# Performance work log

Hardware: AMD Instinct MI355X
Metric: run time of the kernel (lower is better)

Reference implementation:

```python
import jax, jax.numpy as jnp
import numpy as np

NEG_SLOPE = 0.2
EPS = 1e-16  # PyG softmax eps


def _gat_conv(x, src, dst, W, att_src, att_dst, bias, heads, out_ch):
    """PyG GATConv (eval mode, self-loops already appended, concat output)."""
    N = x.shape[0]
    xw = (x @ W).reshape(N, heads, out_ch)            # [N,H,C]
    a_src = jnp.sum(xw * att_src, axis=-1)            # [N,H]
    a_dst = jnp.sum(xw * att_dst, axis=-1)            # [N,H]
    e = jax.nn.leaky_relu(a_src[src] + a_dst[dst], NEG_SLOPE)  # [E,H]
    m = jax.ops.segment_max(e, dst, num_segments=N)   # [N,H] (self-loops -> no empty segs)
    e = jnp.exp(e - m[dst])
    denom = jax.ops.segment_sum(e, dst, num_segments=N)
    alpha = e / (denom[dst] + EPS)                    # [E,H]
    msg = xw[src] * alpha[:, :, None]                 # [E,H,C]
    out = jax.ops.segment_sum(msg, dst, num_segments=N)  # [N,H,C]
    return out.reshape(N, heads * out_ch) + bias


def setup_inputs() -> dict:
    key = jax.random.key(0)
    ks = jax.random.split(key, 12)
    N, E, F_in, H, C, NC = 20000, 320000, 512, 8, 64, 32
    x = jax.random.normal(ks[0], (N, F_in), dtype=jnp.float32)
    edge_index = jax.random.randint(ks[1], (2, E), 0, N, dtype=jnp.int64)
    g = lambda k, shape, fan: jax.random.normal(k, shape, dtype=jnp.float32) * (1.0 / np.sqrt(fan))
    return {
        "x": x,
        "edge_index": edge_index,
        "W1": g(ks[2], (F_in, H * C), F_in),
        "att_src1": g(ks[3], (H, C), C),
        "att_dst1": g(ks[4], (H, C), C),
        "b1": jnp.zeros((H * C,), dtype=jnp.float32),
        "W2": g(ks[5], (H * C, NC), H * C),
        "att_src2": g(ks[6], (1, NC), NC),
        "att_dst2": g(ks[7], (1, NC), NC),
        "b2": jnp.zeros((NC,), dtype=jnp.float32),
    }


def reference(x, edge_index, W1, att_src1, att_dst1, b1, W2, att_src2, att_dst2, b2):
    N = x.shape[0]
    H, C = att_src1.shape
    NC = att_src2.shape[1]
    # GATConv adds self-loops by default
    loops = jnp.arange(N, dtype=edge_index.dtype)
    src = jnp.concatenate([edge_index[0], loops])
    dst = jnp.concatenate([edge_index[1], loops])
    h = _gat_conv(x, src, dst, W1, att_src1, att_dst1, b1, H, C)
    h = jax.nn.elu(h)
    h = _gat_conv(h, src, dst, W2, att_src2, att_dst2, b2, 1, NC)
    return jax.nn.log_softmax(h, axis=1)
```

## Files before the change

kernel.cpp:

```cpp
#include <hip/hip_runtime.h>
#include <math.h>

#define NEG_SLOPE 0.2f
#define SM_EPS 1e-16f

typedef short short8 __attribute__((ext_vector_type(8)));
typedef float floatx4 __attribute__((ext_vector_type(4)));


__device__ inline unsigned short f2bf(float x) {
    unsigned int u = __float_as_uint(x);
    unsigned int r = (u + 0x7FFFu + ((u >> 16) & 1u)) >> 16;
    return (unsigned short)r;
}

__device__ inline float bf2f(unsigned short h) {
    return __uint_as_float(((unsigned int)h) << 16);
}

__device__ inline float bflo(unsigned int u) { return __uint_as_float(u << 16); }
__device__ inline float bfhi(unsigned int u) { return __uint_as_float(u & 0xFFFF0000u); }

__device__ __forceinline__ void gl_lds16(const unsigned short* g, unsigned short* l) {
    __builtin_amdgcn_global_load_lds(
        (const __attribute__((address_space(1))) unsigned int*)(g),
        (__attribute__((address_space(3))) unsigned int*)(l), 16, 0, 0);
}

__device__ inline void get_edge(const int* __restrict__ srcA, const int* __restrict__ dstA,
                                int e, int E, int& s, int& d) {
    if (e < E) { s = srcA[e]; d = dstA[e]; }
    else { s = e - E; d = e - E; }
}


__global__ __launch_bounds__(256) void k_prep(const float* __restrict__ x,
                                              unsigned short* __restrict__ xb,
                                              const float* __restrict__ W1,
                                              unsigned short* __restrict__ w1t,
                                              const float* __restrict__ W2,
                                              unsigned short* __restrict__ w2bt,
                                              const int* __restrict__ dstA,
                                              int E, int Ep,
                                              int* __restrict__ deg,
                                              int nblk_deg, int nblk_x) {
    __shared__ float tile[32][33];
    int bx = blockIdx.x;
    int t = threadIdx.x;
    if (bx < nblk_deg) {
        int e = bx * 256 + t;
        if (e < Ep) {
            int d = (e < E) ? dstA[e] : (e - E);
            atomicAdd(&deg[d], 1);
        }
    } else if (bx < nblk_deg + nblk_x) {
        int i = ((bx - nblk_deg) * 256 + t) * 4;
        float4 v = *(const float4*)(x + i);
        ushort4 o;
        o.x = f2bf(v.x); o.y = f2bf(v.y); o.z = f2bf(v.z); o.w = f2bf(v.w);
        *(ushort4*)(xb + i) = o;
    } else if (bx < nblk_deg + nblk_x + 256) {
        int b = bx - nblk_deg - nblk_x;
        int kb = (b & 15) * 32;
        int nb = (b >> 4) * 32;
        int tx = t & 31, ty = t >> 5;
        #pragma unroll
        for (int i = 0; i < 32; i += 8)
            tile[ty + i][tx] = W1[(size_t)(kb + ty + i) * 512 + nb + tx];
        __syncthreads();
        #pragma unroll
        for (int i = 0; i < 32; i += 8)
            w1t[(size_t)(nb + ty + i) * 512 + kb + tx] = f2bf(tile[tx][ty + i]);
    } else {
        int i = (bx - nblk_deg - nblk_x - 256) * 256 + t;
        int c = i >> 9, k = i & 511;
        w2bt[i] = f2bf(W2[k * 32 + c]);
    }
}


__global__ __launch_bounds__(256) void k_scan_fused(const int* __restrict__ deg,
                                                    int* __restrict__ part,
                                                    int* __restrict__ done,
                                                    int* __restrict__ off,
                                                    int* __restrict__ cursor,
                                                    int N, int nblk) {
    __shared__ int sm[256];
    int bx = blockIdx.x, t = threadIdx.x;
    int i = bx * 256 + t;
    int v = (i < N) ? deg[i] : 0;
    sm[t] = v; __syncthreads();
    for (int o = 1; o < 256; o <<= 1) {
        int x = (t >= o) ? sm[t - o] : 0;
        __syncthreads();
        sm[t] += x;
        __syncthreads();
    }
    int incl_v = sm[t];
    if (t == 255) {
        part[bx] = sm[255];
        __threadfence();
        atomicAdd(done, 1);
    }
    if (t == 0) {
        while (atomicAdd(done, 0) < nblk) { }
        __threadfence();
    }
    __syncthreads();
    int partial = 0;
    for (int j = t; j < bx; j += 256) partial += atomicAdd(&part[j], 0);
    sm[t] = partial; __syncthreads();
    for (int o = 128; o > 0; o >>= 1) {
        if (t < o) sm[t] += sm[t + o];
        __syncthreads();
    }
    int base = sm[0];
    if (i < N) {
        int vv = incl_v + base;
        off[i + 1] = vv;
        cursor[i] = vv - v;
        if (i == 0) off[0] = 0;
    }
}

__global__ __launch_bounds__(256) void k_scatter(const int* __restrict__ srcA, const int* __restrict__ dstA,
                                                 int E, int Ep, int* __restrict__ cursor,
                                                 int* __restrict__ src_s) {
    int e = blockIdx.x * 256 + threadIdx.x;
    if (e >= Ep) return;
    int s, d; get_edge(srcA, dstA, e, E, s, d);
    int p = atomicAdd(&cursor[d], 1);
    src_s[p] = s;
}


__global__ __launch_bounds__(256, 4) void k_gemm1_mfma(const unsigned short* __restrict__ A,
                                                       const unsigned short* __restrict__ Bt,
                                                       const float* __restrict__ att_s,
                                                       const float* __restrict__ att_d,
                                                       unsigned short* __restrict__ C,
                                                       float* __restrict__ a_sd,
                                                       float* __restrict__ a_dd, int M) {
    const int K = 512;
    __shared__ unsigned short As[2][64 * 32];
    __shared__ unsigned short Bs[2][128 * 32];
    int t = threadIdx.x;
    int lane = t & 63;
    int w = t >> 6;
    int row0 = blockIdx.x * 64;
    int col0 = blockIdx.y * 128;
    int wm = (w >> 1) * 32, wn = (w & 1) * 64;
    int l15 = lane & 15, q = lane >> 4;

    int srl = lane >> 2;
    int sgc = ((lane & 3) ^ ((lane >> 3) & 3)) * 8;

    floatx4 acc[2][4] = {};

    auto STAGE = [&](int buf, int k0) {
        gl_lds16(A  + (size_t)(row0 + w * 16 + srl) * K + k0 + sgc, &As[buf][(w * 16) * 32]);
        gl_lds16(Bt + (size_t)(col0 + w * 32 + srl) * K + k0 + sgc, &Bs[buf][(w * 32) * 32]);
        gl_lds16(Bt + (size_t)(col0 + w * 32 + 16 + srl) * K + k0 + sgc, &Bs[buf][(w * 32 + 16) * 32]);
    };

    STAGE(0, 0);
    asm volatile("s_waitcnt vmcnt(0)" ::: "memory");
    __builtin_amdgcn_s_barrier();

    int swz = (l15 >> 1) & 3;
    int buf = 0;
    for (int k0 = 0; k0 < K; k0 += 32) {
        if (k0 + 32 < K) {
            STAGE(buf ^ 1, k0 + 32);
            asm volatile("s_waitcnt vmcnt(3)" ::: "memory");
        } else {
            asm volatile("s_waitcnt vmcnt(0)" ::: "memory");
        }
        __builtin_amdgcn_s_barrier();
        __builtin_amdgcn_sched_barrier(0);
        short8 af[2], bfr[4];
        int sw = (q ^ swz) << 3;
        #pragma unroll
        for (int i = 0; i < 2; ++i)
            af[i] = *(const short8*)(&As[buf][(wm + i * 16 + l15) * 32 + sw]);
        #pragma unroll
        for (int j = 0; j < 4; ++j)
            bfr[j] = *(const short8*)(&Bs[buf][(wn + j * 16 + l15) * 32 + sw]);
        #pragma unroll
        for (int i = 0; i < 2; ++i)
            #pragma unroll
            for (int j = 0; j < 4; ++j)
                acc[i][j] = __builtin_amdgcn_mfma_f32_16x16x32_bf16(af[i], bfr[j], acc[i][j], 0, 0, 0);
        asm volatile("s_waitcnt lgkmcnt(0)" ::: "memory");
        __builtin_amdgcn_sched_barrier(0);
        __builtin_amdgcn_s_barrier();
        buf ^= 1;
    }

    #pragma unroll
    for (int i = 0; i < 2; ++i) {
        #pragma unroll
        for (int p = 0; p < 4; ++p) {
            int r = row0 + wm + i * 16 + q * 4 + p;
            if (r < M) {
                #pragma unroll
                for (int j = 0; j < 4; ++j) {
                    int c = col0 + wn + j * 16 + l15;
                    C[(size_t)r * 512 + c] = f2bf(acc[i][j][p]);
                }
            }
        }
    }

    int hh = blockIdx.y * 2 + (w & 1);
    float asr[4], adr[4];
    #pragma unroll
    for (int j = 0; j < 4; ++j) {
        asr[j] = att_s[hh * 64 + j * 16 + l15];
        adr[j] = att_d[hh * 64 + j * 16 + l15];
    }
    #pragma unroll
    for (int i = 0; i < 2; ++i) {
        #pragma unroll
        for (int p = 0; p < 4; ++p) {
            float ds = 0.f, dd = 0.f;
            #pragma unroll
            for (int j = 0; j < 4; ++j) {
                ds = fmaf(acc[i][j][p], asr[j], ds);
                dd = fmaf(acc[i][j][p], adr[j], dd);
            }
            #pragma unroll
            for (int mk = 1; mk <= 8; mk <<= 1) {
                ds += __shfl_xor(ds, mk);
                dd += __shfl_xor(dd, mk);
            }
            int r = row0 + wm + i * 16 + q * 4 + p;
            if (l15 == 0 && r < M) {
                a_sd[(size_t)hh * M + r] = ds;
                a_dd[(size_t)hh * M + r] = dd;
            }
        }
    }
}


__global__ __launch_bounds__(256) void k_l1(const unsigned short* __restrict__ xw,
                                            const float* __restrict__ a_s,
                                            const float* __restrict__ a_d,
                                            const int* __restrict__ off,
                                            const int* __restrict__ src_s,
                                            const float* __restrict__ bias,
                                            unsigned short* __restrict__ hout, int N) {
    int wid = threadIdx.x >> 6, lane = threadIdx.x & 63;
    int h = blockIdx.x & 7;
    int n = (blockIdx.x >> 3) * 32 + wid * 8 + (lane >> 3);
    int li = lane & 7;
    if (n >= N) return;
    int p0 = off[n], p1 = off[n + 1];
    const float* ash = a_s + (size_t)h * N;
    float adv = a_d[(size_t)h * N + n];
    const size_t cbase = (size_t)h * 64 + (size_t)li * 8;

    float acc[8] = {};
    float s = 0.f;
    int p = p0;
    if (p + 4 <= p1) {
        int s0 = src_s[p], s1 = src_s[p + 1], s2 = src_s[p + 2], s3 = src_s[p + 3];
        while (true) {
            const uint4 u0 = *(const uint4*)(xw + (size_t)s0 * 512 + cbase);
            const uint4 u1 = *(const uint4*)(xw + (size_t)s1 * 512 + cbase);
            const uint4 u2 = *(const uint4*)(xw + (size_t)s2 * 512 + cbase);
            const uint4 u3 = *(const uint4*)(xw + (size_t)s3 * 512 + cbase);
            float e0 = ash[s0] + adv; e0 = e0 > 0.f ? e0 : NEG_SLOPE * e0;
            float e1 = ash[s1] + adv; e1 = e1 > 0.f ? e1 : NEG_SLOPE * e1;
            float e2 = ash[s2] + adv; e2 = e2 > 0.f ? e2 : NEG_SLOPE * e2;
            float e3 = ash[s3] + adv; e3 = e3 > 0.f ? e3 : NEG_SLOPE * e3;
            int np = p + 4;
            bool more = (np + 4 <= p1);
            int t0 = 0, t1 = 0, t2 = 0, t3 = 0;
            if (more) {
                t0 = src_s[np]; t1 = src_s[np + 1];
                t2 = src_s[np + 2]; t3 = src_s[np + 3];
            }
            float w0 = __expf(e0);
            float w1 = __expf(e1);
            float w2 = __expf(e2);
            float w3 = __expf(e3);
            s += (w0 + w1) + (w2 + w3);
            acc[0] = fmaf(w0, bflo(u0.x), acc[0]); acc[1] = fmaf(w0, bfhi(u0.x), acc[1]);
            acc[2] = fmaf(w0, bflo(u0.y), acc[2]); acc[3] = fmaf(w0, bfhi(u0.y), acc[3]);
            acc[4] = fmaf(w0, bflo(u0.z), acc[4]); acc[5] = fmaf(w0, bfhi(u0.z), acc[5]);
            acc[6] = fmaf(w0, bflo(u0.w), acc[6]); acc[7] = fmaf(w0, bfhi(u0.w), acc[7]);
            acc[0] = fmaf(w1, bflo(u1.x), acc[0]); acc[1] = fmaf(w1, bfhi(u1.x), acc[1]);
            acc[2] = fmaf(w1, bflo(u1.y), acc[2]); acc[3] = fmaf(w1, bfhi(u1.y), acc[3]);
            acc[4] = fmaf(w1, bflo(u1.z), acc[4]); acc[5] = fmaf(w1, bfhi(u1.z), acc[5]);
            acc[6] = fmaf(w1, bflo(u1.w), acc[6]); acc[7] = fmaf(w1, bfhi(u1.w), acc[7]);
            acc[0] = fmaf(w2, bflo(u2.x), acc[0]); acc[1] = fmaf(w2, bfhi(u2.x), acc[1]);
            acc[2] = fmaf(w2, bflo(u2.y), acc[2]); acc[3] = fmaf(w2, bfhi(u2.y), acc[3]);
            acc[4] = fmaf(w2, bflo(u2.z), acc[4]); acc[5] = fmaf(w2, bfhi(u2.z), acc[5]);
            acc[6] = fmaf(w2, bflo(u2.w), acc[6]); acc[7] = fmaf(w2, bfhi(u2.w), acc[7]);
            acc[0] = fmaf(w3, bflo(u3.x), acc[0]); acc[1] = fmaf(w3, bfhi(u3.x), acc[1]);
            acc[2] = fmaf(w3, bflo(u3.y), acc[2]); acc[3] = fmaf(w3, bfhi(u3.y), acc[3]);
            acc[4] = fmaf(w3, bflo(u3.z), acc[4]); acc[5] = fmaf(w3, bfhi(u3.z), acc[5]);
            acc[6] = fmaf(w3, bflo(u3.w), acc[6]); acc[7] = fmaf(w3, bfhi(u3.w), acc[7]);
            p = np;
            if (!more) break;
            s0 = t0; s1 = t1; s2 = t2; s3 = t3;
        }
    }
    for (; p < p1; ++p) {
        int s0 = src_s[p];
        const uint4 u0 = *(const uint4*)(xw + (size_t)s0 * 512 + cbase);
        float e0 = ash[s0] + adv; e0 = e0 > 0.f ? e0 : NEG_SLOPE * e0;
        float w0 = __expf(e0);
        s += w0;
        acc[0] = fmaf(w0, bflo(u0.x), acc[0]); acc[1] = fmaf(w0, bfhi(u0.x), acc[1]);
        acc[2] = fmaf(w0, bflo(u0.y), acc[2]); acc[3] = fmaf(w0, bfhi(u0.y), acc[3]);
        acc[4] = fmaf(w0, bflo(u0.z), acc[4]); acc[5] = fmaf(w0, bfhi(u0.z), acc[5]);
        acc[6] = fmaf(w0, bflo(u0.w), acc[6]); acc[7] = fmaf(w0, bfhi(u0.w), acc[7]);
    }

    float inv = 1.f / (s + SM_EPS);
    unsigned int ov[4];
    #pragma unroll
    for (int j = 0; j < 4; ++j) {
        float v0 = acc[2 * j] * inv     + bias[cbase + 2 * j];
        float v1 = acc[2 * j + 1] * inv + bias[cbase + 2 * j + 1];
        v0 = v0 > 0.f ? v0 : __expf(v0) - 1.f;
        v1 = v1 > 0.f ? v1 : __expf(v1) - 1.f;
        ov[j] = (unsigned int)f2bf(v0) | ((unsigned int)f2bf(v1) << 16);
    }
    *(uint4*)(hout + (size_t)n * 512 + cbase) = make_uint4(ov[0], ov[1], ov[2], ov[3]);
}


__global__ __launch_bounds__(256) void k_gemm2_mfma(const unsigned short* __restrict__ A,
                                                    const unsigned short* __restrict__ Bt,
                                                    const float* __restrict__ att_s,
                                                    const float* __restrict__ att_d,
                                                    unsigned short* __restrict__ O,
                                                    float* __restrict__ a_s, float* __restrict__ a_d,
                                                    int M) {
    const int K = 512;
    __shared__ unsigned short As[64 * 512];
    __shared__ unsigned short Bs[32 * 512];
    int t = threadIdx.x;
    int lane = t & 63;
    int w = t >> 6;
    int row0 = blockIdx.x * 64;
    int l15 = lane & 15, q = lane >> 4;

    #pragma unroll
    for (int i = 0; i < 16; ++i) {
        int r = w * 16 + i;
        gl_lds16(A + (size_t)(row0 + r) * K + ((lane ^ (r & 7)) << 3), &As[r * 512]);
    }
    #pragma unroll
    for (int i = 0; i < 8; ++i) {
        int r = w * 8 + i;
        gl_lds16(Bt + (size_t)r * K + ((lane ^ (r & 7)) << 3), &Bs[r * 512]);
    }
    __syncthreads();

    floatx4 acc[2] = {};
    int ra = w * 16 + l15;
    int rb0 = l15, rb1 = 16 + l15;
    #pragma unroll
    for (int k0 = 0; k0 < K; k0 += 32) {
        int cc = (k0 >> 3) + q;
        short8 af = *(const short8*)(&As[ra * 512 + ((cc ^ (ra & 7)) << 3)]);
        short8 b0 = *(const short8*)(&Bs[rb0 * 512 + ((cc ^ (rb0 & 7)) << 3)]);
        short8 b1 = *(const short8*)(&Bs[rb1 * 512 + ((cc ^ (rb1 & 7)) << 3)]);
        acc[0] = __builtin_amdgcn_mfma_f32_16x16x32_bf16(af, b0, acc[0], 0, 0, 0);
        acc[1] = __builtin_amdgcn_mfma_f32_16x16x32_bf16(af, b1, acc[1], 0, 0, 0);
    }

    float as_lo = att_s[l15], as_hi = att_s[16 + l15];
    float ad_lo = att_d[l15], ad_hi = att_d[16 + l15];
    #pragma unroll
    for (int p = 0; p < 4; ++p) {
        int r = row0 + w * 16 + q * 4 + p;
        bool ok = r < M;
        float v0 = acc[0][p], v1 = acc[1][p];
        if (ok) {
            O[(size_t)r * 32 + l15]      = f2bf(v0);
            O[(size_t)r * 32 + 16 + l15] = f2bf(v1);
        }
        float ds = v0 * as_lo + v1 * as_hi;
        float dd = v0 * ad_lo + v1 * ad_hi;
        #pragma unroll
        for (int mk = 1; mk <= 8; mk <<= 1) {
            ds += __shfl_xor(ds, mk);
            dd += __shfl_xor(dd, mk);
        }
        if (ok && l15 == 0) { a_s[r] = ds; a_d[r] = dd; }
    }
}


__global__ __launch_bounds__(256) void k_l2(const unsigned short* __restrict__ hw2,
                                            const float* __restrict__ a_s,
                                            const float* __restrict__ a_d,
                                            const int* __restrict__ off,
                                            const int* __restrict__ src_s,
                                            const float* __restrict__ bias,
                                            float* __restrict__ outp, int N) {
    int wid = threadIdx.x >> 6, lane = threadIdx.x & 63;
    int n = blockIdx.x * 4 + wid;
    if (n >= N) return;
    int p0 = off[n], p1 = off[n + 1];
    float adv = a_d[n];
    int e8 = lane >> 3;
    int li = lane & 7;
    const int cbase = li * 4;

    float acc[4] = {};
    float s = 0.f;
    int p = p0;
    for (; p + 16 <= p1; p += 16) {
        int sA = src_s[p + e8];
        int sB = src_s[p + 8 + e8];
        const uint2 uA = *(const uint2*)(hw2 + (size_t)sA * 32 + cbase);
        const uint2 uB = *(const uint2*)(hw2 + (size_t)sB * 32 + cbase);
        float eA = a_s[sA] + adv; eA = eA > 0.f ? eA : NEG_SLOPE * eA;
        float eB = a_s[sB] + adv; eB = eB > 0.f ? eB : NEG_SLOPE * eB;
        float wA = __expf(eA);
        float wB = __expf(eB);
        s += wA + wB;
        acc[0] = fmaf(wA, bflo(uA.x), acc[0]); acc[1] = fmaf(wA, bfhi(uA.x), acc[1]);
        acc[2] = fmaf(wA, bflo(uA.y), acc[2]); acc[3] = fmaf(wA, bfhi(uA.y), acc[3]);
        acc[0] = fmaf(wB, bflo(uB.x), acc[0]); acc[1] = fmaf(wB, bfhi(uB.x), acc[1]);
        acc[2] = fmaf(wB, bflo(uB.y), acc[2]); acc[3] = fmaf(wB, bfhi(uB.y), acc[3]);
    }
    for (; p + 8 <= p1; p += 8) {
        int sA = src_s[p + e8];
        const uint2 uA = *(const uint2*)(hw2 + (size_t)sA * 32 + cbase);
        float eA = a_s[sA] + adv; eA = eA > 0.f ? eA : NEG_SLOPE * eA;
        float wA = __expf(eA);
        s += wA;
        acc[0] = fmaf(wA, bflo(uA.x), acc[0]); acc[1] = fmaf(wA, bfhi(uA.x), acc[1]);
        acc[2] = fmaf(wA, bflo(uA.y), acc[2]); acc[3] = fmaf(wA, bfhi(uA.y), acc[3]);
    }
    if (p < p1) {
        int nb = p1 - p;
        bool val = e8 < nb;
        int sA = src_s[val ? p + e8 : p];
        const uint2 uA = *(const uint2*)(hw2 + (size_t)sA * 32 + cbase);
        float eA = a_s[sA] + adv; eA = eA > 0.f ? eA : NEG_SLOPE * eA;
        float wA = val ? __expf(eA) : 0.f;
        s += wA;
        acc[0] = fmaf(wA, bflo(uA.x), acc[0]); acc[1] = fmaf(wA, bfhi(uA.x), acc[1]);
        acc[2] = fmaf(wA, bflo(uA.y), acc[2]); acc[3] = fmaf(wA, bfhi(uA.y), acc[3]);
    }

    #pragma unroll
    for (int mk = 8; mk <= 32; mk <<= 1) {
        s += __shfl_xor(s, mk);
        #pragma unroll
        for (int j = 0; j < 4; ++j) acc[j] += __shfl_xor(acc[j], mk);
    }

    float inv = 1.f / (s + SM_EPS);
    float v[4];
    #pragma unroll
    for (int j = 0; j < 4; ++j) v[j] = acc[j] * inv + bias[cbase + j];

    float mx = fmaxf(fmaxf(v[0], v[1]), fmaxf(v[2], v[3]));
    mx = fmaxf(mx, __shfl_xor(mx, 1));
    mx = fmaxf(mx, __shfl_xor(mx, 2));
    mx = fmaxf(mx, __shfl_xor(mx, 4));
    float sum = 0.f;
    #pragma unroll
    for (int j = 0; j < 4; ++j) sum += __expf(v[j] - mx);
    sum += __shfl_xor(sum, 1);
    sum += __shfl_xor(sum, 2);
    sum += __shfl_xor(sum, 4);
    float lse = __logf(sum);
    if (e8 == 0) {
        float4 o = make_float4(v[0] - mx - lse, v[1] - mx - lse,
                               v[2] - mx - lse, v[3] - mx - lse);
        *(float4*)(outp + (size_t)n * 32 + cbase) = o;
    }
}


extern "C" void kernel_launch(void* const* d_in, const int* in_sizes, int n_in,
                              void* d_out, int out_size, void* d_ws, size_t ws_size,
                              hipStream_t stream) {
    const float* x   = (const float*)d_in[0];
    const int*   ei  = (const int*)d_in[1];
    const float* W1  = (const float*)d_in[2];
    const float* as1 = (const float*)d_in[3];
    const float* ad1 = (const float*)d_in[4];
    const float* b1  = (const float*)d_in[5];
    const float* W2  = (const float*)d_in[6];
    const float* as2 = (const float*)d_in[7];
    const float* ad2 = (const float*)d_in[8];
    const float* b2  = (const float*)d_in[9];
    float* out = (float*)d_out;

    const int F = 512;
    const int N = in_sizes[0] / F;
    const int E = in_sizes[1] / 2;
    const int Ep = E + N;
    const int* srcA = ei;
    const int* dstA = ei + E;

    char* w = (char*)d_ws;
    auto alloc = [&](size_t b) -> void* {
        void* p = (void*)w;
        w += (b + 255) & ~(size_t)255;
        return p;
    };
    unsigned short* xbf  = (unsigned short*)alloc((size_t)N * 512 * 2);
    unsigned short* w1t  = (unsigned short*)alloc((size_t)512 * 512 * 2);
    unsigned short* w2bt = (unsigned short*)alloc((size_t)32 * 512 * 2);
    unsigned short* xw1  = (unsigned short*)alloc((size_t)N * 512 * 2);
    unsigned short* hbuf = (unsigned short*)alloc((size_t)N * 512 * 2);
    float* a_s1 = (float*)alloc((size_t)N * 8 * 4);
    float* a_d1 = (float*)alloc((size_t)N * 8 * 4);
    unsigned short* hw2 = (unsigned short*)alloc((size_t)N * 32 * 2);
    float* a_s2 = (float*)alloc((size_t)N * 4);
    float* a_d2 = (float*)alloc((size_t)N * 4);
    int* deg    = (int*)alloc((size_t)N * 4);
    int* done   = (int*)alloc(256);
    int* incl   = (int*)alloc((size_t)N * 4);
    int* part   = (int*)alloc(256 * 4);
    int* off    = (int*)alloc((size_t)(N + 1) * 4);
    int* cursor = (int*)alloc((size_t)N * 4);
    int* src_s  = (int*)alloc((size_t)Ep * 4);
    (void)incl;

    int egrid = (Ep + 255) / 256;
    int sgrid = (N + 255) / 256;
    int ngrid4 = (N + 3) / 4;
    int nblk_x = (N * 512 / 4) / 256;
    int nblk_w2 = (32 * 512 + 255) / 256;

    hipMemsetAsync(deg, 0, (((size_t)N * 4 + 255) & ~(size_t)255) + 256, stream);

    k_prep<<<egrid + nblk_x + 256 + nblk_w2, 256, 0, stream>>>(
        x, xbf, W1, w1t, W2, w2bt, dstA, E, Ep, deg, egrid, nblk_x);

    k_scan_fused<<<sgrid, 256, 0, stream>>>(deg, part, done, off, cursor, N, sgrid);
    k_scatter<<<egrid, 256, 0, stream>>>(srcA, dstA, E, Ep, cursor, src_s);

    {
        dim3 g1((N + 63) / 64, 512 / 128);
        k_gemm1_mfma<<<g1, 256, 0, stream>>>(xbf, w1t, as1, ad1, xw1, a_s1, a_d1, N);
    }
    {
        int ngrid32 = (N + 31) / 32;
        k_l1<<<ngrid32 * 8, 256, 0, stream>>>(xw1, a_s1, a_d1, off, src_s, b1, hbuf, N);
    }

    k_gemm2_mfma<<<(N + 63) / 64, 256, 0, stream>>>(hbuf, w2bt, as2, ad2, hw2, a_s2, a_d2, N);
    k_l2<<<ngrid4, 256, 0, stream>>>(hw2, a_s2, a_d2, off, src_s, b2, out, N);
}
```

Measured before the change: 224.1 us.

## Split layer-1 edge aggregation across eight lane groups per node with shuffle reduction

The layer-1 aggregation kernel now gives each wavefront one (node, head) pair instead of eight nodes. The eight 8-lane groups each take a different edge of the neighbour list, and the partial sums are merged with xor shuffles before one group writes the output. This is meant to raise memory-level parallelism and cut the serial per-edge loop length, which with about 17 edges per node becomes roughly two iterations. In exchange it launches eight times more blocks, adds 27 cross-lane shuffles per thread, and leaves most lanes idle in the store and in the masked tail.

```diff
diff --git a/kernel.cpp b/kernel.cpp
--- a/kernel.cpp
+++ b/kernel.cpp
@@ -253,9 +253,10 @@
                                             unsigned short* __restrict__ hout, int N) {
     int wid = threadIdx.x >> 6, lane = threadIdx.x & 63;
     int h = blockIdx.x & 7;
-    int n = (blockIdx.x >> 3) * 32 + wid * 8 + (lane >> 3);
+    int n = (blockIdx.x >> 3) * 4 + wid;
+    if (n >= N) return;
+    int e8 = lane >> 3;
     int li = lane & 7;
-    if (n >= N) return;
     int p0 = off[n], p1 = off[n + 1];
     const float* ash = a_s + (size_t)h * N;
     float adv = a_d[(size_t)h * N + n];
@@ -264,60 +265,55 @@
     float acc[8] = {};
     float s = 0.f;
     int p = p0;
-    if (p + 4 <= p1) {
-        int s0 = src_s[p], s1 = src_s[p + 1], s2 = src_s[p + 2], s3 = src_s[p + 3];
-        while (true) {
-            const uint4 u0 = *(const uint4*)(xw + (size_t)s0 * 512 + cbase);
-            const uint4 u1 = *(const uint4*)(xw + (size_t)s1 * 512 + cbase);
-            const uint4 u2 = *(const uint4*)(xw + (size_t)s2 * 512 + cbase);
-            const uint4 u3 = *(const uint4*)(xw + (size_t)s3 * 512 + cbase);
-            float e0 = ash[s0] + adv; e0 = e0 > 0.f ? e0 : NEG_SLOPE * e0;
-            float e1 = ash[s1] + adv; e1 = e1 > 0.f ? e1 : NEG_SLOPE * e1;
-            float e2 = ash[s2] + adv; e2 = e2 > 0.f ? e2 : NEG_SLOPE * e2;
-            float e3 = ash[s3] + adv; e3 = e3 > 0.f ? e3 : NEG_SLOPE * e3;
-            int np = p + 4;
-            bool more = (np + 4 <= p1);
-            int t0 = 0, t1 = 0, t2 = 0, t3 = 0;
-            if (more) {
-                t0 = src_s[np]; t1 = src_s[np + 1];
-                t2 = src_s[np + 2]; t3 = src_s[np + 3];
-            }
-            float w0 = __expf(e0);
-            float w1 = __expf(e1);
-            float w2 = __expf(e2);
-            float w3 = __expf(e3);
-            s += (w0 + w1) + (w2 + w3);
-            acc[0] = fmaf(w0, bflo(u0.x), acc[0]); acc[1] = fmaf(w0, bfhi(u0.x), acc[1]);
-            acc[2] = fmaf(w0, bflo(u0.y), acc[2]); acc[3] = fmaf(w0, bfhi(u0.y), acc[3]);
-            acc[4] = fmaf(w0, bflo(u0.z), acc[4]); acc[5] = fmaf(w0, bfhi(u0.z), acc[5]);
-            acc[6] = fmaf(w0, bflo(u0.w), acc[6]); acc[7] = fmaf(w0, bfhi(u0.w), acc[7]);
-            acc[0] = fmaf(w1, bflo(u1.x), acc[0]); acc[1] = fmaf(w1, bfhi(u1.x), acc[1]);
-            acc[2] = fmaf(w1, bflo(u1.y), acc[2]); acc[3] = fmaf(w1, bfhi(u1.y), acc[3]);
-            acc[4] = fmaf(w1, bflo(u1.z), acc[4]); acc[5] = fmaf(w1, bfhi(u1.z), acc[5]);
-            acc[6] = fmaf(w1, bflo(u1.w), acc[6]); acc[7] = fmaf(w1, bfhi(u1.w), acc[7]);
-            acc[0] = fmaf(w2, bflo(u2.x), acc[0]); acc[1] = fmaf(w2, bfhi(u2.x), acc[1]);
-            acc[2] = fmaf(w2, bflo(u2.y), acc[2]); acc[3] = fmaf(w2, bfhi(u2.y), acc[3]);
-            acc[4] = fmaf(w2, bflo(u2.z), acc[4]); acc[5] = fmaf(w2, bfhi(u2.z), acc[5]);
-            acc[6] = fmaf(w2, bflo(u2.w), acc[6]); acc[7] = fmaf(w2, bfhi(u2.w), acc[7]);
-            acc[0] = fmaf(w3, bflo(u3.x), acc[0]); acc[1] = fmaf(w3, bfhi(u3.x), acc[1]);
-            acc[2] = fmaf(w3, bflo(u3.y), acc[2]); acc[3] = fmaf(w3, bfhi(u3.y), acc[3]);
-            acc[4] = fmaf(w3, bflo(u3.z), acc[4]); acc[5] = fmaf(w3, bfhi(u3.z), acc[5]);
-            acc[6] = fmaf(w3, bflo(u3.w), acc[6]); acc[7] = fmaf(w3, bfhi(u3.w), acc[7]);
-            p = np;
-            if (!more) break;
-            s0 = t0; s1 = t1; s2 = t2; s3 = t3;
-        }
-    }
-    for (; p < p1; ++p) {
-        int s0 = src_s[p];
-        const uint4 u0 = *(const uint4*)(xw + (size_t)s0 * 512 + cbase);
-        float e0 = ash[s0] + adv; e0 = e0 > 0.f ? e0 : NEG_SLOPE * e0;
-        float w0 = __expf(e0);
-        s += w0;
-        acc[0] = fmaf(w0, bflo(u0.x), acc[0]); acc[1] = fmaf(w0, bfhi(u0.x), acc[1]);
-        acc[2] = fmaf(w0, bflo(u0.y), acc[2]); acc[3] = fmaf(w0, bfhi(u0.y), acc[3]);
-        acc[4] = fmaf(w0, bflo(u0.z), acc[4]); acc[5] = fmaf(w0, bfhi(u0.z), acc[5]);
-        acc[6] = fmaf(w0, bflo(u0.w), acc[6]); acc[7] = fmaf(w0, bfhi(u0.w), acc[7]);
+    for (; p + 16 <= p1; p += 16) {
+        int sA = src_s[p + e8];
+        int sB = src_s[p + 8 + e8];
+        const uint4 uA = *(const uint4*)(xw + (size_t)sA * 512 + cbase);
+        const uint4 uB = *(const uint4*)(xw + (size_t)sB * 512 + cbase);
+        float eA = ash[sA] + adv; eA = eA > 0.f ? eA : NEG_SLOPE * eA;
+        float eB = ash[sB] + adv; eB = eB > 0.f ? eB : NEG_SLOPE * eB;
+        float wA = __expf(eA);
+        float wB = __expf(eB);
+        s += wA + wB;
+        acc[0] = fmaf(wA, bflo(uA.x), acc[0]); acc[1] = fmaf(wA, bfhi(uA.x), acc[1]);
+        acc[2] = fmaf(wA, bflo(uA.y), acc[2]); acc[3] = fmaf(wA, bfhi(uA.y), acc[3]);
+        acc[4] = fmaf(wA, bflo(uA.z), acc[4]); acc[5] = fmaf(wA, bfhi(uA.z), acc[5]);
+        acc[6] = fmaf(wA, bflo(uA.w), acc[6]); acc[7] = fmaf(wA, bfhi(uA.w), acc[7]);
+        acc[0] = fmaf(wB, bflo(uB.x), acc[0]); acc[1] = fmaf(wB, bfhi(uB.x), acc[1]);
+        acc[2] = fmaf(wB, bflo(uB.y), acc[2]); acc[3] = fmaf(wB, bfhi(uB.y), acc[3]);
+        acc[4] = fmaf(wB, bflo(uB.z), acc[4]); acc[5] = fmaf(wB, bfhi(uB.z), acc[5]);
+        acc[6] = fmaf(wB, bflo(uB.w), acc[6]); acc[7] = fmaf(wB, bfhi(uB.w), acc[7]);
+    }
+    for (; p + 8 <= p1; p += 8) {
+        int sA = src_s[p + e8];
+        const uint4 uA = *(const uint4*)(xw + (size_t)sA * 512 + cbase);
+        float eA = ash[sA] + adv; eA = eA > 0.f ? eA : NEG_SLOPE * eA;
+        float wA = __expf(eA);
+        s += wA;
+        acc[0] = fmaf(wA, bflo(uA.x), acc[0]); acc[1] = fmaf(wA, bfhi(uA.x), acc[1]);
+        acc[2] = fmaf(wA, bflo(uA.y), acc[2]); acc[3] = fmaf(wA, bfhi(uA.y), acc[3]);
+        acc[4] = fmaf(wA, bflo(uA.z), acc[4]); acc[5] = fmaf(wA, bfhi(uA.z), acc[5]);
+        acc[6] = fmaf(wA, bflo(uA.w), acc[6]); acc[7] = fmaf(wA, bfhi(uA.w), acc[7]);
+    }
+    if (p < p1) {
+        int nb = p1 - p;
+        bool val = e8 < nb;
+        int sA = src_s[val ? p + e8 : p];
+        const uint4 uA = *(const uint4*)(xw + (size_t)sA * 512 + cbase);
+        float eA = ash[sA] + adv; eA = eA > 0.f ? eA : NEG_SLOPE * eA;
+        float wA = val ? __expf(eA) : 0.f;
+        s += wA;
+        acc[0] = fmaf(wA, bflo(uA.x), acc[0]); acc[1] = fmaf(wA, bfhi(uA.x), acc[1]);
+        acc[2] = fmaf(wA, bflo(uA.y), acc[2]); acc[3] = fmaf(wA, bfhi(uA.y), acc[3]);
+        acc[4] = fmaf(wA, bflo(uA.z), acc[4]); acc[5] = fmaf(wA, bfhi(uA.z), acc[5]);
+        acc[6] = fmaf(wA, bflo(uA.w), acc[6]); acc[7] = fmaf(wA, bfhi(uA.w), acc[7]);
+    }
+
+    #pragma unroll
+    for (int mk = 8; mk <= 32; mk <<= 1) {
+        s += __shfl_xor(s, mk);
+        #pragma unroll
+        for (int j = 0; j < 8; ++j) acc[j] += __shfl_xor(acc[j], mk);
     }
 
     float inv = 1.f / (s + SM_EPS);
@@ -330,7 +326,8 @@
         v1 = v1 > 0.f ? v1 : __expf(v1) - 1.f;
         ov[j] = (unsigned int)f2bf(v0) | ((unsigned int)f2bf(v1) << 16);
     }
-    *(uint4*)(hout + (size_t)n * 512 + cbase) = make_uint4(ov[0], ov[1], ov[2], ov[3]);
+    if (e8 == 0)
+        *(uint4*)(hout + (size_t)n * 512 + cbase) = make_uint4(ov[0], ov[1], ov[2], ov[3]);
 }
 
 
@@ -550,8 +547,8 @@
         k_gemm1_mfma<<<g1, 256, 0, stream>>>(xbf, w1t, as1, ad1, xw1, a_s1, a_d1, N);
     }
     {
-        int ngrid32 = (N + 31) / 32;
-        k_l1<<<ngrid32 * 8, 256, 0, stream>>>(xw1, a_s1, a_d1, off, src_s, b1, hbuf, N);
+        int nblk_l1 = ((N + 3) / 4) * 8;
+        k_l1<<<nblk_l1, 256, 0, stream>>>(xw1, a_s1, a_d1, off, src_s, b1, hbuf, N);
     }
 
     k_gemm2_mfma<<<(N + 63) / 64, 256, 0, stream>>>(hbuf, w2bt, as2, ad2, hw2, a_s2, a_d2, N);
```

Measured after the change: 252.2 us. +12.6%, slower.
